# Kernel tuning notes

Measured on AMD Instinct MI355X. Metric: run time of the kernel, lower is better.

## Reference

```python
import jax, jax.numpy as jnp
import numpy as np
import math

EPS = 1e-5
BN_SCALE = 1.0 / math.sqrt(1.0 + EPS)  # eval BatchNorm with running mean 0, var 1


def _ln(x, g, b):
    m = jnp.mean(x, axis=-1, keepdims=True)
    v = jnp.mean((x - m) ** 2, axis=-1, keepdims=True)
    return (x - m) * jax.lax.rsqrt(v + EPS) * g + b


def _swish(x):
    return x * jax.nn.sigmoid(x)


def _ffn(x, ng, nb, w1, b1, w2, b2):
    h = _ln(x, ng, nb)
    h = _swish(h @ w1.T + b1)
    return h @ w2.T + b2


def _mhsa(x, a_ng, a_nb, qkv_w, qkv_b, rel_w, out_w, out_b):
    B, T, D = x.shape
    H, hd = rel_w.shape  # rel_pos_proj: Linear(head_dim, num_heads), weight [H, hd]
    h = _ln(x, a_ng, a_nb)
    qkv = (h @ qkv_w.T + qkv_b).reshape(B, T, 3, H, hd)
    q = qkv[:, :, 0].transpose(0, 2, 1, 3)  # [B,H,T,hd]
    k = qkv[:, :, 1].transpose(0, 2, 1, 3)
    v = qkv[:, :, 2].transpose(0, 2, 1, 3)
    scores = jnp.einsum('bhqd,bhkd->bhqk', q, k) * (hd ** -0.5)
    # relative sinusoidal PE over 2T-1 offsets
    pos = jnp.arange(-(T - 1), T, dtype=x.dtype)[:, None]
    div = jnp.exp(jnp.arange(0, hd, 2, dtype=x.dtype) * (-math.log(10000.0) / hd))
    ang = pos * div  # [2T-1, hd/2]
    pe = jnp.zeros((2 * T - 1, hd), dtype=x.dtype)
    pe = pe.at[:, 0::2].set(jnp.sin(ang)).at[:, 1::2].set(jnp.cos(ang))
    rel_bias = pe @ rel_w.T  # [2T-1, H]
    idx = jnp.arange(T)[:, None] - jnp.arange(T)[None, :] + (T - 1)  # [T,T]
    bias = rel_bias[idx].transpose(2, 0, 1)  # [H,T,T]
    attn = jax.nn.softmax(scores + bias[None], axis=-1)
    o = jnp.einsum('bhqk,bhkd->bhqd', attn, v).transpose(0, 2, 1, 3).reshape(B, T, D)
    return o @ out_w.T + out_b


def _conv(x, c_ng, c_nb, pw1_w, pw1_b, dw_w, dw_b, bn_g, bn_b, pw2_w, pw2_b):
    B, T, D = x.shape
    K = dw_w.shape[1]
    h = _ln(x, c_ng, c_nb)
    h = h @ pw1_w.T + pw1_b  # pointwise conv == linear, [B,T,2D]
    a, g = jnp.split(h, 2, axis=-1)
    h = a * jax.nn.sigmoid(g)  # GLU, [B,T,D]
    h = h.transpose(0, 2, 1)  # [B,D,T]
    h = jax.lax.conv_general_dilated(
        h, dw_w[:, None, :], window_strides=(1,), padding=[(K // 2, K // 2)],
        dimension_numbers=('NCH', 'OIH', 'NCH'), feature_group_count=D) + dw_b[:, None]
    h = h * (BN_SCALE * bn_g)[:, None] + bn_b[:, None]  # eval-mode BatchNorm1d
    h = _swish(h)
    h = h.transpose(0, 2, 1)  # [B,T,D]
    return h @ pw2_w.T + pw2_b


def _forward(x, g_ffn1, b_ffn1, g_mhsa, b_mhsa, g_conv, b_conv, g_ffn2, b_ffn2, g_out, b_out,
             f1_ng, f1_nb, f1_w1, f1_b1, f1_w2, f1_b2,
             f2_ng, f2_nb, f2_w1, f2_b1, f2_w2, f2_b2,
             a_ng, a_nb, qkv_w, qkv_b, rel_w, out_w, out_b,
             c_ng, c_nb, pw1_w, pw1_b, dw_w, dw_b, bn_g, bn_b, pw2_w, pw2_b):
    x = x + 0.5 * _ffn(_ln(x, g_ffn1, b_ffn1), f1_ng, f1_nb, f1_w1, f1_b1, f1_w2, f1_b2)
    x = x + _mhsa(_ln(x, g_mhsa, b_mhsa), a_ng, a_nb, qkv_w, qkv_b, rel_w, out_w, out_b)
    x = x + _conv(_ln(x, g_conv, b_conv), c_ng, c_nb, pw1_w, pw1_b, dw_w, dw_b, bn_g, bn_b, pw2_w, pw2_b)
    x = _ln(x + 0.5 * _ffn(_ln(x, g_ffn2, b_ffn2), f2_ng, f2_nb, f2_w1, f2_b1, f2_w2, f2_b2), g_out, b_out)
    return x


def setup_inputs() -> dict:
    key = jax.random.key(0)
    B, T, D, H, F, K = 8, 2048, 256, 4, 1024, 31
    ks = iter(jax.random.split(key, 16))
    w = lambda shape, s: jax.random.normal(next(ks), shape, jnp.float32) * s
    d = {}
    d['x'] = w((B, T, D), 1.0)
    for n in ['g_ffn1', 'g_mhsa', 'g_conv', 'g_ffn2', 'g_out', 'f1_ng', 'f2_ng', 'a_ng', 'c_ng', 'bn_g']:
        d[n] = jnp.ones((D,), jnp.float32)
    for n in ['b_ffn1', 'b_mhsa', 'b_conv', 'b_ffn2', 'b_out', 'f1_nb', 'f2_nb', 'a_nb', 'c_nb', 'bn_b']:
        d[n] = jnp.zeros((D,), jnp.float32)
    d['f1_w1'] = w((F, D), 0.05); d['f1_b1'] = jnp.zeros((F,), jnp.float32)
    d['f1_w2'] = w((D, F), 0.03); d['f1_b2'] = jnp.zeros((D,), jnp.float32)
    d['f2_w1'] = w((F, D), 0.05); d['f2_b1'] = jnp.zeros((F,), jnp.float32)
    d['f2_w2'] = w((D, F), 0.03); d['f2_b2'] = jnp.zeros((D,), jnp.float32)
    d['qkv_w'] = w((3 * D, D), 0.05); d['qkv_b'] = jnp.zeros((3 * D,), jnp.float32)
    d['rel_w'] = w((H, D // H), 0.05)
    d['out_w'] = w((D, D), 0.05); d['out_b'] = jnp.zeros((D,), jnp.float32)
    d['pw1_w'] = w((2 * D, D), 0.05); d['pw1_b'] = jnp.zeros((2 * D,), jnp.float32)
    d['dw_w'] = w((D, K), 0.1); d['dw_b'] = jnp.zeros((D,), jnp.float32)
    d['pw2_w'] = w((D, D), 0.05); d['pw2_b'] = jnp.zeros((D,), jnp.float32)
    return d


def reference(x, g_ffn1, b_ffn1, g_mhsa, b_mhsa, g_conv, b_conv, g_ffn2, b_ffn2, g_out, b_out,
              f1_ng, f1_nb, f1_w1, f1_b1, f1_w2, f1_b2,
              f2_ng, f2_nb, f2_w1, f2_b1, f2_w2, f2_b2,
              a_ng, a_nb, qkv_w, qkv_b, rel_w, out_w, out_b,
              c_ng, c_nb, pw1_w, pw1_b, dw_w, dw_b, bn_g, bn_b, pw2_w, pw2_b):
    return _forward(x, g_ffn1, b_ffn1, g_mhsa, b_mhsa, g_conv, b_conv, g_ffn2, b_ffn2, g_out, b_out,
                    f1_ng, f1_nb, f1_w1, f1_b1, f1_w2, f1_b2,
                    f2_ng, f2_nb, f2_w1, f2_b1, f2_w2, f2_b2,
                    a_ng, a_nb, qkv_w, qkv_b, rel_w, out_w, out_b,
                    c_ng, c_nb, pw1_w, pw1_b, dw_w, dw_b, bn_g, bn_b, pw2_w, pw2_b)
```

## Files before the change

### kernel.cpp

```cpp
#include <hip/hip_runtime.h>
#include <math.h>


typedef _Float16 half8 __attribute__((ext_vector_type(8)));
typedef _Float16 half4v __attribute__((ext_vector_type(4)));
typedef float floatx4 __attribute__((ext_vector_type(4)));

#define LN_EPS 1e-5f
#define BN_SCALE 0.9999950000374996f
#define LOG2E 1.44269504f
#define QSCALE (0.125f * LOG2E)

__device__ __forceinline__ void async_copy16(const _Float16* g, _Float16* l) {
    __builtin_amdgcn_global_load_lds(
        (const __attribute__((address_space(1))) void*)g,
        (__attribute__((address_space(3))) void*)l, 16, 0, 0);
}

struct CastJobs { const float* s[7]; _Float16* d[7]; };
__global__ __launch_bounds__(256) void cast_all(CastJobs j) {
    int i = blockIdx.x * 256 + threadIdx.x;
    int seg, base;
    if (i < 1048576)      { seg = i >> 18; base = seg << 18; }
    else if (i < 1245184) { seg = 4; base = 1048576; }
    else if (i < 1310720) { seg = 5; base = 1245184; }
    else                  { seg = 6; base = 1310720; }
    j.d[seg][i - base] = (_Float16)j.s[seg][i - base];
}

__global__ __launch_bounds__(256) void cast_pw1_kernel(const float* __restrict__ w,
        const float* __restrict__ b, _Float16* __restrict__ wp, float* __restrict__ bp) {
    int i = blockIdx.x * 256 + threadIdx.x;
    int p = i >> 8, c = i & 255;
    int chunk = p >> 4, within = p & 15;
    int orig = ((chunk & 1) ? 256 : 0) + (chunk >> 1) * 16 + within;
    wp[i] = (_Float16)w[orig * 256 + c];
    if (c == 0) bp[p] = b[orig];
}

__global__ __launch_bounds__(256) void ln2_kernel(const float* __restrict__ x,
        const float* __restrict__ g1, const float* __restrict__ b1,
        const float* __restrict__ g2, const float* __restrict__ b2,
        _Float16* __restrict__ y) {
    int wave = threadIdx.x >> 6, lane = threadIdx.x & 63;
    size_t row = (size_t)blockIdx.x * 4 + wave;
    float4 v = ((const float4*)(x + row * 256))[lane];
    float s = v.x + v.y + v.z + v.w;
    float s2 = v.x * v.x + v.y * v.y + v.z * v.z + v.w * v.w;
    #pragma unroll
    for (int m = 1; m < 64; m <<= 1) { s += __shfl_xor(s, m, 64); s2 += __shfl_xor(s2, m, 64); }
    float mean = s * (1.f / 256.f);
    float var = s2 * (1.f / 256.f) - mean * mean;
    float rs = rsqrtf(var + LN_EPS);
    int c0 = lane * 4;
    float y0 = (v.x - mean) * rs * g1[c0 + 0] + b1[c0 + 0];
    float y1 = (v.y - mean) * rs * g1[c0 + 1] + b1[c0 + 1];
    float y2 = (v.z - mean) * rs * g1[c0 + 2] + b1[c0 + 2];
    float y3 = (v.w - mean) * rs * g1[c0 + 3] + b1[c0 + 3];
    float t = y0 + y1 + y2 + y3;
    float t2 = y0 * y0 + y1 * y1 + y2 * y2 + y3 * y3;
    #pragma unroll
    for (int m = 1; m < 64; m <<= 1) { t += __shfl_xor(t, m, 64); t2 += __shfl_xor(t2, m, 64); }
    float mean2 = t * (1.f / 256.f);
    float var2 = t2 * (1.f / 256.f) - mean2 * mean2;
    float rs2 = rsqrtf(var2 + LN_EPS);
    half4v o;
    o[0] = (_Float16)((y0 - mean2) * rs2 * g2[c0 + 0] + b2[c0 + 0]);
    o[1] = (_Float16)((y1 - mean2) * rs2 * g2[c0 + 1] + b2[c0 + 1]);
    o[2] = (_Float16)((y2 - mean2) * rs2 * g2[c0 + 2] + b2[c0 + 2]);
    o[3] = (_Float16)((y3 - mean2) * rs2 * g2[c0 + 3] + b2[c0 + 3]);
    *(half4v*)(y + row * 256 + c0) = o;
}

__global__ __launch_bounds__(256) void ln1_kernel(const float* __restrict__ x,
        const float* __restrict__ g, const float* __restrict__ b,
        float* __restrict__ y) {
    int wave = threadIdx.x >> 6, lane = threadIdx.x & 63;
    size_t row = (size_t)blockIdx.x * 4 + wave;
    float4 v = ((const float4*)(x + row * 256))[lane];
    float s = v.x + v.y + v.z + v.w;
    float s2 = v.x * v.x + v.y * v.y + v.z * v.z + v.w * v.w;
    #pragma unroll
    for (int m = 1; m < 64; m <<= 1) { s += __shfl_xor(s, m, 64); s2 += __shfl_xor(s2, m, 64); }
    float mean = s * (1.f / 256.f);
    float var = s2 * (1.f / 256.f) - mean * mean;
    float rs = rsqrtf(var + LN_EPS);
    int c0 = lane * 4;
    float4 o;
    o.x = (v.x - mean) * rs * g[c0 + 0] + b[c0 + 0];
    o.y = (v.y - mean) * rs * g[c0 + 1] + b[c0 + 1];
    o.z = (v.z - mean) * rs * g[c0 + 2] + b[c0 + 2];
    o.w = (v.w - mean) * rs * g[c0 + 3] + b[c0 + 3];
    ((float4*)(y + row * 256))[lane] = o;
}

template <int EPI>
__global__ __launch_bounds__(256) void gemm128(
        const _Float16* __restrict__ A, const _Float16* __restrict__ W,
        const float* __restrict__ bias, const float* __restrict__ res, float alpha,
        float* __restrict__ outf, _Float16* __restrict__ outh,
        _Float16* __restrict__ outv, int N, int K) {
    __shared__ _Float16 As[128 * 64];
    __shared__ _Float16 Ws[128 * 64];
    int tid = threadIdx.x, wave = tid >> 6, lane = tid & 63;
    int n0 = blockIdx.x * 128, m0 = blockIdx.y * 128;
    int wr = wave >> 1, wc = wave & 1;
    floatx4 acc[4][4] = {};
    int l15 = lane & 15, kq = (lane >> 4) * 8, quad = lane >> 4;
    int srow = wave * 32 + (lane >> 3);
    int scol = (lane & 7) * 8;
    const _Float16* Aptr = A + (size_t)(m0 + srow) * K + scol;
    const _Float16* Wptr = W + (size_t)(n0 + srow) * K + scol;
    _Float16* AsBase = As + wave * 32 * 64;
    _Float16* WsBase = Ws + wave * 32 * 64;
    for (int k0 = 0; k0 < K; k0 += 64) {
        __syncthreads();
        #pragma unroll
        for (int i = 0; i < 4; i++)
            async_copy16(Aptr + k0 + (size_t)i * 8 * K, AsBase + i * 8 * 64);
        #pragma unroll
        for (int i = 0; i < 4; i++)
            async_copy16(Wptr + k0 + (size_t)i * 8 * K, WsBase + i * 8 * 64);
        __syncthreads();
        #pragma unroll
        for (int ks = 0; ks < 2; ks++) {
            half8 a[4], b[4];
            #pragma unroll
            for (int i = 0; i < 4; i++)
                a[i] = *(const half8*)&As[(wr * 64 + i * 16 + l15) * 64 + ks * 32 + kq];
            #pragma unroll
            for (int j = 0; j < 4; j++)
                b[j] = *(const half8*)&Ws[(wc * 64 + j * 16 + l15) * 64 + ks * 32 + kq];
            #pragma unroll
            for (int i = 0; i < 4; i++)
                #pragma unroll
                for (int j = 0; j < 4; j++)
                    acc[i][j] = __builtin_amdgcn_mfma_f32_16x16x32_f16(a[i], b[j], acc[i][j], 0, 0, 0);
        }
    }
    #pragma unroll
    for (int i = 0; i < 4; i++) {
        int mrow = m0 + wr * 64 + i * 16 + quad * 4;
        if (EPI == 2) {
            #pragma unroll
            for (int jp = 0; jp < 2; jp++) {
                int j = 2 * jp;
                int Pa = n0 + wc * 64 + j * 16 + l15;
                float ba = bias[Pa], bg = bias[Pa + 16];
                int d = ((Pa >> 5) << 4) + l15;
                #pragma unroll
                for (int r = 0; r < 4; r++) {
                    float av = acc[i][j][r] + ba;
                    float gv = acc[i][j + 1][r] + bg;
                    outh[(size_t)(mrow + r) * 256 + d] = (_Float16)(av / (1.f + __expf(-gv)));
                }
            }
        } else if (EPI == 5) {
            float qs = (n0 < 256) ? QSCALE : 1.f;
            #pragma unroll
            for (int j = 0; j < 4; j++) {
                int n = n0 + wc * 64 + j * 16 + l15;
                float bv = bias[n];
                if (n0 < 512) {
                    #pragma unroll
                    for (int r = 0; r < 4; r++)
                        outh[(size_t)(mrow + r) * N + n] = (_Float16)((acc[i][j][r] + bv) * qs);
                } else {
                    int hv = (n - 512) >> 6, d = (n - 512) & 63;
                    int bb = m0 >> 11;
                    int t0 = (m0 & 2047) + wr * 64 + i * 16 + quad * 4;
                    half4v vv;
                    #pragma unroll
                    for (int r = 0; r < 4; r++) vv[r] = (_Float16)(acc[i][j][r] + bv);
                    *(half4v*)(outv + ((size_t)((bb * 4 + hv) * 64 + d)) * 2048 + t0) = vv;
                }
            }
        } else {
            #pragma unroll
            for (int j = 0; j < 4; j++) {
                int n = n0 + wc * 64 + j * 16 + l15;
                float bv = bias[n];
                #pragma unroll
                for (int r = 0; r < 4; r++) {
                    float c = acc[i][j][r] + bv;
                    size_t m = (size_t)(mrow + r);
                    if (EPI == 1) {
                        outh[m * N + n] = (_Float16)(c / (1.f + __expf(-c)));
                    } else {
                        outf[m * N + n] = res[m * N + n] + alpha * c;
                    }
                }
            }
        }
    }
}

__global__ __launch_bounds__(256) void relbias_kernel(const float* __restrict__ rel_w,
                                                      float* __restrict__ rb) {
    int i = blockIdx.x * 256 + threadIdx.x;
    if (i >= 4095 * 4) return;
    int p = i >> 2, h = i & 3;
    float pos = (float)(p - 2047);
    const float c = -logf(10000.f) / 64.f;
    float acc = 0.f;
    for (int k = 0; k < 32; k++) {
        float dv = expf((float)(2 * k) * c);
        float ang = pos * dv;
        acc += sinf(ang) * rel_w[h * 64 + 2 * k] + cosf(ang) * rel_w[h * 64 + 2 * k + 1];
    }
    rb[h * 4095 + p] = acc * LOG2E;
}

__global__ __launch_bounds__(256) void attn_kernel(const _Float16* __restrict__ qkv,
        const _Float16* __restrict__ vtg, const float* __restrict__ rb,
        _Float16* __restrict__ o) {
    const int T = 2048;
    int qt = blockIdx.x, h = blockIdx.y, b = blockIdx.z;
    int tid = threadIdx.x, wave = tid >> 6, lane = tid & 63;
    __shared__ __align__(16) _Float16 PQ[128 * 72];
    __shared__ __align__(16) _Float16 Ks[64][72];
    __shared__ __align__(16) _Float16 Vt[64][72];
    __shared__ __align__(16) float bias4[4][192];
    auto Qs = (_Float16(*)[72])PQ;
    auto Ps = (_Float16(*)[32][72])PQ;

    int l15 = lane & 15, quad = lane >> 4, kq = quad * 8;
    size_t qrow0 = (size_t)b * T + qt * 128;
    #pragma unroll
    for (int i = 0; i < 4; i++) {
        int idx = tid + 256 * i, r = idx >> 3, sg = idx & 7;
        *(float4*)(&Qs[r][sg * 8]) = *(const float4*)(qkv + (qrow0 + r) * 768 + h * 64 + sg * 8);
    }
    __syncthreads();
    half8 qa[2][2];
    #pragma unroll
    for (int u = 0; u < 2; u++)
        #pragma unroll
        for (int ks = 0; ks < 2; ks++)
            qa[u][ks] = *(const half8*)(&Qs[u * 64 + wave * 16 + l15][ks * 32 + kq]);
    half8 ones;
    #pragma unroll
    for (int j = 0; j < 8; j++) ones[j] = (_Float16)1.f;

    floatx4 oacc[2][4] = {};
    floatx4 lacc[2] = {};
    const float* rbh = rb + h * 4095;
    const _Float16* vbase = vtg + ((size_t)(b * 4 + h)) * 64 * 2048;
    const _Float16* kbase = qkv + ((size_t)b * T) * 768 + 256 + h * 64;
    int cshift = (63 - l15) & 3;

    for (int kt = 0; kt < 32; kt++) {
        __syncthreads();
        #pragma unroll
        for (int i = 0; i < 2; i++) {
            int idx = tid + 256 * i, r = idx >> 3, sg = idx & 7;
            *(float4*)(&Ks[r][sg * 8]) = *(const float4*)(kbase + (size_t)(kt * 64 + r) * 768 + sg * 8);
            *(float4*)(&Vt[r][sg * 8]) = *(const float4*)(vbase + (size_t)r * 2048 + kt * 64 + sg * 8);
        }
        if (tid < 192) {
            int base = qt * 128 - kt * 64 + 1984;
            float v = rbh[min(base + tid, 4094)];
            #pragma unroll
            for (int c = 0; c < 4; c++) {
                int idx = tid - c;
                if (idx >= 0) bias4[c][idx] = v;
            }
        }
        __syncthreads();
        half8 kf[2][4];
        #pragma unroll
        for (int ks = 0; ks < 2; ks++)
            #pragma unroll
            for (int nt = 0; nt < 4; nt++)
                kf[ks][nt] = *(const half8*)(&Ks[nt * 16 + l15][ks * 32 + kq]);
        floatx4 s[2][4];
        #pragma unroll
        for (int u = 0; u < 2; u++)
            #pragma unroll
            for (int nt = 0; nt < 4; nt++) {
                int cb = u * 64 + wave * 16 + quad * 4 - (nt * 16 + l15) + 63;
                s[u][nt] = *(const floatx4*)&bias4[cshift][cb - cshift];
            }
        #pragma unroll
        for (int u = 0; u < 2; u++)
            #pragma unroll
            for (int ks = 0; ks < 2; ks++)
                #pragma unroll
                for (int nt = 0; nt < 4; nt++)
                    s[u][nt] = __builtin_amdgcn_mfma_f32_16x16x32_f16(qa[u][ks], kf[ks][nt], s[u][nt], 0, 0, 0);
        #pragma unroll
        for (int u = 0; u < 2; u++)
            #pragma unroll
            for (int nt = 0; nt < 4; nt++)
                #pragma unroll
                for (int r = 0; r < 4; r++)
                    Ps[wave][u * 16 + quad * 4 + r][nt * 16 + l15] =
                        (_Float16)__builtin_amdgcn_exp2f(fminf(s[u][nt][r], 15.86f));
        half8 vf[2][4];
        #pragma unroll
        for (int ks = 0; ks < 2; ks++)
            #pragma unroll
            for (int nt = 0; nt < 4; nt++)
                vf[ks][nt] = *(const half8*)(&Vt[nt * 16 + l15][ks * 32 + kq]);
        #pragma unroll
        for (int u = 0; u < 2; u++)
            #pragma unroll
            for (int ks = 0; ks < 2; ks++) {
                half8 pa = *(const half8*)(&Ps[wave][u * 16 + l15][ks * 32 + kq]);
                lacc[u] = __builtin_amdgcn_mfma_f32_16x16x32_f16(pa, ones, lacc[u], 0, 0, 0);
                #pragma unroll
                for (int nt = 0; nt < 4; nt++)
                    oacc[u][nt] = __builtin_amdgcn_mfma_f32_16x16x32_f16(pa, vf[ks][nt], oacc[u][nt], 0, 0, 0);
            }
    }
    #pragma unroll
    for (int u = 0; u < 2; u++) {
        size_t orow0 = qrow0 + u * 64 + wave * 16 + quad * 4;
        #pragma unroll
        for (int r = 0; r < 4; r++) {
            float inv = 1.f / lacc[u][r];
            #pragma unroll
            for (int nt = 0; nt < 4; nt++)
                o[(orow0 + r) * 256 + h * 64 + nt * 16 + l15] = (_Float16)(oacc[u][nt][r] * inv);
        }
    }
}

__global__ __launch_bounds__(256) void dwconv_kernel(const _Float16* __restrict__ glu,
        const float* __restrict__ dw_w, const float* __restrict__ dw_b,
        const float* __restrict__ bn_g, const float* __restrict__ bn_b,
        _Float16* __restrict__ out) {
    const int T = 2048;
    int d = threadIdx.x;
    int b = blockIdx.y, t0 = blockIdx.x * 128;
    const _Float16* base = glu + ((size_t)b * T) * 256 + d;
    float w[31], win[31];
    #pragma unroll
    for (int j = 0; j < 31; j++) w[j] = dw_w[d * 31 + j];
    #pragma unroll
    for (int j = 0; j < 31; j++) {
        int tt = t0 - 15 + j;
        win[j] = (tt >= 0 && tt < T) ? (float)base[(size_t)tt * 256] : 0.f;
    }
    float dwb = dw_b[d];
    float bns = BN_SCALE * bn_g[d];
    float bnb = bn_b[d];
    size_t orow = ((size_t)b * T) * 256 + d;
    for (int i = 0; i < 128; i++) {
        int t = t0 + i;
        float acc = dwb;
        #pragma unroll
        for (int j = 0; j < 31; j++) acc += win[j] * w[j];
        float bn = acc * bns + bnb;
        out[orow + (size_t)t * 256] = (_Float16)(bn / (1.f + __expf(-bn)));
        #pragma unroll
        for (int j = 0; j < 30; j++) win[j] = win[j + 1];
        int tn = t + 16;
        win[30] = (tn < T) ? (float)base[(size_t)tn * 256] : 0.f;
    }
}

extern "C" void kernel_launch(void* const* d_in, const int* in_sizes, int n_in,
                              void* d_out, int out_size, void* d_ws, size_t ws_size,
                              hipStream_t stream) {
    (void)in_sizes; (void)n_in; (void)out_size; (void)ws_size;
    const float* x      = (const float*)d_in[0];
    const float* g_ffn1 = (const float*)d_in[1];
    const float* g_mhsa = (const float*)d_in[2];
    const float* g_conv = (const float*)d_in[3];
    const float* g_ffn2 = (const float*)d_in[4];
    const float* g_out  = (const float*)d_in[5];
    const float* f1_ng  = (const float*)d_in[6];
    const float* f2_ng  = (const float*)d_in[7];
    const float* a_ng   = (const float*)d_in[8];
    const float* c_ng   = (const float*)d_in[9];
    const float* bn_g   = (const float*)d_in[10];
    const float* b_ffn1 = (const float*)d_in[11];
    const float* b_mhsa = (const float*)d_in[12];
    const float* b_conv = (const float*)d_in[13];
    const float* b_ffn2 = (const float*)d_in[14];
    const float* b_out  = (const float*)d_in[15];
    const float* f1_nb  = (const float*)d_in[16];
    const float* f2_nb  = (const float*)d_in[17];
    const float* a_nb   = (const float*)d_in[18];
    const float* c_nb   = (const float*)d_in[19];
    const float* bn_b   = (const float*)d_in[20];
    const float* f1_w1  = (const float*)d_in[21];
    const float* f1_b1  = (const float*)d_in[22];
    const float* f1_w2  = (const float*)d_in[23];
    const float* f1_b2  = (const float*)d_in[24];
    const float* f2_w1  = (const float*)d_in[25];
    const float* f2_b1  = (const float*)d_in[26];
    const float* f2_w2  = (const float*)d_in[27];
    const float* f2_b2  = (const float*)d_in[28];
    const float* qkv_w  = (const float*)d_in[29];
    const float* qkv_b  = (const float*)d_in[30];
    const float* rel_w  = (const float*)d_in[31];
    const float* out_w  = (const float*)d_in[32];
    const float* out_b  = (const float*)d_in[33];
    const float* pw1_w  = (const float*)d_in[34];
    const float* pw1_b  = (const float*)d_in[35];
    const float* dw_w   = (const float*)d_in[36];
    const float* dw_b   = (const float*)d_in[37];
    const float* pw2_w  = (const float*)d_in[38];
    const float* pw2_b  = (const float*)d_in[39];

    const int BT = 16384;
    char* ws = (char*)d_ws;
    size_t off = 0;
    auto alloc = [&](size_t bytes) -> char* {
        char* p = ws + off;
        off += (bytes + 255) & ~(size_t)255;
        return p;
    };
    _Float16* wf1w1 = (_Float16*)alloc(262144 * 2);
    _Float16* wf1w2 = (_Float16*)alloc(262144 * 2);
    _Float16* wf2w1 = (_Float16*)alloc(262144 * 2);
    _Float16* wf2w2 = (_Float16*)alloc(262144 * 2);
    _Float16* wqkv  = (_Float16*)alloc(196608 * 2);
    _Float16* wout  = (_Float16*)alloc(65536 * 2);
    _Float16* wpw1  = (_Float16*)alloc(131072 * 2);
    float* pb1      = (float*)alloc(512 * 4);
    _Float16* wpw2  = (_Float16*)alloc(65536 * 2);
    float* rbbuf    = (float*)alloc(4 * 4095 * 4);
    float* xA       = (float*)alloc((size_t)BT * 256 * 4);
    float* xB       = (float*)alloc((size_t)BT * 256 * 4);
    _Float16* t16   = (_Float16*)alloc((size_t)BT * 256 * 2);
    char* R1        = alloc((size_t)BT * 1024 * 2);
    _Float16* vtg   = (_Float16*)alloc((size_t)8 * 4 * 64 * 2048 * 2);
    _Float16* glu16 = (_Float16*)alloc((size_t)BT * 256 * 2);
    _Float16* o16   = (_Float16*)alloc((size_t)BT * 256 * 2);
    _Float16* h16   = (_Float16*)R1;
    _Float16* qkv16 = (_Float16*)R1;

    CastJobs cj;
    cj.s[0] = f1_w1; cj.d[0] = wf1w1;
    cj.s[1] = f1_w2; cj.d[1] = wf1w2;
    cj.s[2] = f2_w1; cj.d[2] = wf2w1;
    cj.s[3] = f2_w2; cj.d[3] = wf2w2;
    cj.s[4] = qkv_w; cj.d[4] = wqkv;
    cj.s[5] = out_w; cj.d[5] = wout;
    cj.s[6] = pw2_w; cj.d[6] = wpw2;
    cast_all<<<5376, 256, 0, stream>>>(cj);
    cast_pw1_kernel<<<512, 256, 0, stream>>>(pw1_w, pw1_b, wpw1, pb1);
    relbias_kernel<<<64, 256, 0, stream>>>(rel_w, rbbuf);

    ln2_kernel<<<BT / 4, 256, 0, stream>>>(x, g_ffn1, b_ffn1, f1_ng, f1_nb, t16);
    gemm128<1><<<dim3(8, 128), 256, 0, stream>>>(t16, wf1w1, f1_b1, nullptr, 0.f, nullptr, h16, nullptr, 1024, 256);
    gemm128<3><<<dim3(2, 128), 256, 0, stream>>>(h16, wf1w2, f1_b2, x, 0.5f, xA, nullptr, nullptr, 256, 1024);
    ln2_kernel<<<BT / 4, 256, 0, stream>>>(xA, g_mhsa, b_mhsa, a_ng, a_nb, t16);
    gemm128<5><<<dim3(6, 128), 256, 0, stream>>>(t16, wqkv, qkv_b, nullptr, 0.f, nullptr, qkv16, vtg, 768, 256);
    attn_kernel<<<dim3(16, 4, 8), 256, 0, stream>>>(qkv16, vtg, rbbuf, o16);
    gemm128<3><<<dim3(2, 128), 256, 0, stream>>>(o16, wout, out_b, xA, 1.f, xB, nullptr, nullptr, 256, 256);
    ln2_kernel<<<BT / 4, 256, 0, stream>>>(xB, g_conv, b_conv, c_ng, c_nb, t16);
    gemm128<2><<<dim3(4, 128), 256, 0, stream>>>(t16, wpw1, pb1, nullptr, 0.f, nullptr, glu16, nullptr, 512, 256);
    dwconv_kernel<<<dim3(16, 8), 256, 0, stream>>>(glu16, dw_w, dw_b, bn_g, bn_b, t16);
    gemm128<3><<<dim3(2, 128), 256, 0, stream>>>(t16, wpw2, pw2_b, xB, 1.f, xA, nullptr, nullptr, 256, 256);
    ln2_kernel<<<BT / 4, 256, 0, stream>>>(xA, g_ffn2, b_ffn2, f2_ng, f2_nb, t16);
    gemm128<1><<<dim3(8, 128), 256, 0, stream>>>(t16, wf2w1, f2_b1, nullptr, 0.f, nullptr, h16, nullptr, 1024, 256);
    gemm128<3><<<dim3(2, 128), 256, 0, stream>>>(h16, wf2w2, f2_b2, xA, 0.5f, xB, nullptr, nullptr, 256, 1024);
    ln1_kernel<<<BT / 4, 256, 0, stream>>>(xB, g_out, b_out, (float*)d_out);
}
```

Baseline: 521.1 us.

## Split attention over key halves with combine kernel and swizzle P stores

New measurement: 520.2 us. About the same (-0.2%).

```diff
diff --git a/kernel.cpp b/kernel.cpp
--- a/kernel.cpp
+++ b/kernel.cpp
@@ -213,9 +213,9 @@
 
 __global__ __launch_bounds__(256) void attn_kernel(const _Float16* __restrict__ qkv,
         const _Float16* __restrict__ vtg, const float* __restrict__ rb,
-        _Float16* __restrict__ o) {
+        float* __restrict__ opart, float* __restrict__ lpart) {
     const int T = 2048;
-    int qt = blockIdx.x, h = blockIdx.y, b = blockIdx.z;
+    int qt = blockIdx.x & 15, ksp = blockIdx.x >> 4, h = blockIdx.y, b = blockIdx.z;
     int tid = threadIdx.x, wave = tid >> 6, lane = tid & 63;
     __shared__ __align__(16) _Float16 PQ[128 * 72];
     __shared__ __align__(16) _Float16 Ks[64][72];
@@ -248,8 +248,9 @@
     const _Float16* vbase = vtg + ((size_t)(b * 4 + h)) * 64 * 2048;
     const _Float16* kbase = qkv + ((size_t)b * T) * 768 + 256 + h * 64;
     int cshift = (63 - l15) & 3;
-
-    for (int kt = 0; kt < 32; kt++) {
+    int pswr = (l15 >> 2) << 3;
+
+    for (int kt = ksp * 16; kt < ksp * 16 + 16; kt++) {
         __syncthreads();
         #pragma unroll
         for (int i = 0; i < 2; i++) {
@@ -294,7 +295,7 @@
             for (int nt = 0; nt < 4; nt++)
                 #pragma unroll
                 for (int r = 0; r < 4; r++)
-                    Ps[wave][u * 16 + quad * 4 + r][nt * 16 + l15] =
+                    Ps[wave][u * 16 + quad * 4 + r][(nt * 16 + l15) ^ (quad << 3)] =
                         (_Float16)__builtin_amdgcn_exp2f(fminf(s[u][nt][r], 15.86f));
         half8 vf[2][4];
         #pragma unroll
@@ -306,24 +307,47 @@
         for (int u = 0; u < 2; u++)
             #pragma unroll
             for (int ks = 0; ks < 2; ks++) {
-                half8 pa = *(const half8*)(&Ps[wave][u * 16 + l15][ks * 32 + kq]);
+                half8 pa = *(const half8*)(&Ps[wave][u * 16 + l15][(ks * 32 + kq) ^ pswr]);
                 lacc[u] = __builtin_amdgcn_mfma_f32_16x16x32_f16(pa, ones, lacc[u], 0, 0, 0);
                 #pragma unroll
                 for (int nt = 0; nt < 4; nt++)
                     oacc[u][nt] = __builtin_amdgcn_mfma_f32_16x16x32_f16(pa, vf[ks][nt], oacc[u][nt], 0, 0, 0);
             }
     }
+    float* obase = opart + (size_t)ksp * 16384 * 256;
     #pragma unroll
     for (int u = 0; u < 2; u++) {
         size_t orow0 = qrow0 + u * 64 + wave * 16 + quad * 4;
         #pragma unroll
-        for (int r = 0; r < 4; r++) {
-            float inv = 1.f / lacc[u][r];
+        for (int r = 0; r < 4; r++)
             #pragma unroll
             for (int nt = 0; nt < 4; nt++)
-                o[(orow0 + r) * 256 + h * 64 + nt * 16 + l15] = (_Float16)(oacc[u][nt][r] * inv);
+                obase[(orow0 + r) * 256 + h * 64 + nt * 16 + l15] = oacc[u][nt][r];
+        if (l15 == 0) {
+            int q = qt * 128 + u * 64 + wave * 16 + quad * 4;
+            float* lp = lpart + ksp * 65536 + ((b * 4 + h) << 11) + q;
+            #pragma unroll
+            for (int r = 0; r < 4; r++) lp[r] = lacc[u][r];
         }
     }
+}
+
+__global__ __launch_bounds__(256) void attn_combine(const float* __restrict__ opart,
+        const float* __restrict__ lpart, _Float16* __restrict__ o16) {
+    int wave = threadIdx.x >> 6, lane = threadIdx.x & 63;
+    size_t row = (size_t)blockIdx.x * 4 + wave;
+    int c0 = lane * 4;
+    float4 a = ((const float4*)(opart + row * 256))[lane];
+    float4 bq = ((const float4*)(opart + (size_t)16384 * 256 + row * 256))[lane];
+    int b = (int)(row >> 11), q = (int)(row & 2047), h = c0 >> 6;
+    int li = ((b * 4 + h) << 11) + q;
+    float inv = 1.f / (lpart[li] + lpart[65536 + li]);
+    half4v o;
+    o[0] = (_Float16)((a.x + bq.x) * inv);
+    o[1] = (_Float16)((a.y + bq.y) * inv);
+    o[2] = (_Float16)((a.z + bq.z) * inv);
+    o[3] = (_Float16)((a.w + bq.w) * inv);
+    *(half4v*)(o16 + row * 256 + c0) = o;
 }
 
 __global__ __launch_bounds__(256) void dwconv_kernel(const _Float16* __restrict__ glu,
@@ -428,6 +452,8 @@
     _Float16* t16   = (_Float16*)alloc((size_t)BT * 256 * 2);
     char* R1        = alloc((size_t)BT * 1024 * 2);
     _Float16* vtg   = (_Float16*)alloc((size_t)8 * 4 * 64 * 2048 * 2);
+    float* opart    = (float*)alloc((size_t)2 * BT * 256 * 4);
+    float* lpart    = (float*)alloc((size_t)2 * 65536 * 4);
     _Float16* glu16 = (_Float16*)alloc((size_t)BT * 256 * 2);
     _Float16* o16   = (_Float16*)alloc((size_t)BT * 256 * 2);
     _Float16* h16   = (_Float16*)R1;
@@ -450,7 +476,8 @@
     gemm128<3><<<dim3(2, 128), 256, 0, stream>>>(h16, wf1w2, f1_b2, x, 0.5f, xA, nullptr, nullptr, 256, 1024);
     ln2_kernel<<<BT / 4, 256, 0, stream>>>(xA, g_mhsa, b_mhsa, a_ng, a_nb, t16);
     gemm128<5><<<dim3(6, 128), 256, 0, stream>>>(t16, wqkv, qkv_b, nullptr, 0.f, nullptr, qkv16, vtg, 768, 256);
-    attn_kernel<<<dim3(16, 4, 8), 256, 0, stream>>>(qkv16, vtg, rbbuf, o16);
+    attn_kernel<<<dim3(32, 4, 8), 256, 0, stream>>>(qkv16, vtg, rbbuf, opart, lpart);
+    attn_combine<<<BT / 4, 256, 0, stream>>>(opart, lpart, o16);
     gemm128<3><<<dim3(2, 128), 256, 0, stream>>>(o16, wout, out_b, xA, 1.f, xB, nullptr, nullptr, 256, 256);
     ln2_kernel<<<BT / 4, 256, 0, stream>>>(xB, g_conv, b_conv, c_ng, c_nb, t16);
     gemm128<2><<<dim3(4, 128), 256, 0, stream>>>(t16, wpw1, pb1, nullptr, 0.f, nullptr, glu16, nullptr, 512, 256);
```
